# Optimization experiments

Measured on AMD Instinct MI355X. Metric: run time of the kernel, lower is better.

Reference implementation:

```python
import jax, jax.numpy as jnp
import numpy as np

H = 150  # hidden per direction

def _lstm_dir(x, w_ih, w_hh, b_ih, b_hh):
    # x: [B, T, D] -> hs: [B, T, H]; PyTorch gate order i,f,g,o
    B = x.shape[0]
    xg = jnp.einsum('btd,gd->btg', x, w_ih) + b_ih + b_hh  # precompute input projection [B,T,4H]
    def step(carry, xt):
        h, c = carry
        g = xt + h @ w_hh.T
        i, f, gg, o = jnp.split(g, 4, axis=-1)
        i, f, o = jax.nn.sigmoid(i), jax.nn.sigmoid(f), jax.nn.sigmoid(o)
        c = f * c + i * jnp.tanh(gg)
        h = o * jnp.tanh(c)
        return (h, c), h
    init = (jnp.zeros((B, H), x.dtype), jnp.zeros((B, H), x.dtype))
    _, hs = jax.lax.scan(step, init, jnp.swapaxes(xg, 0, 1))  # [T,B,H]
    return jnp.swapaxes(hs, 0, 1)

def _bilstm(x, w_ih_f, w_hh_f, b_ih_f, b_hh_f, w_ih_b, w_hh_b, b_ih_b, b_hh_b):
    fwd = _lstm_dir(x, w_ih_f, w_hh_f, b_ih_f, b_hh_f)
    bwd = jnp.flip(_lstm_dir(jnp.flip(x, axis=1), w_ih_b, w_hh_b, b_ih_b, b_hh_b), axis=1)
    return jnp.concatenate([fwd, bwd], axis=-1)  # [B, T, 2H]

def setup_inputs() -> dict:
    key = jax.random.key(0)
    ks = jax.random.split(key, 20)
    s = 0.05
    d = {
        'sentences': jax.random.normal(ks[0], (1024, 128, 343), jnp.float32),
        'w_ih_f1': jax.random.normal(ks[1], (600, 343)) * s,
        'w_hh_f1': jax.random.normal(ks[2], (600, 150)) * s,
        'b_ih_f1': jax.random.normal(ks[3], (600,)) * s,
        'b_hh_f1': jax.random.normal(ks[4], (600,)) * s,
        'w_ih_b1': jax.random.normal(ks[5], (600, 343)) * s,
        'w_hh_b1': jax.random.normal(ks[6], (600, 150)) * s,
        'b_ih_b1': jax.random.normal(ks[7], (600,)) * s,
        'b_hh_b1': jax.random.normal(ks[8], (600,)) * s,
        'w_ih_f2': jax.random.normal(ks[9], (600, 300)) * s,
        'w_hh_f2': jax.random.normal(ks[10], (600, 150)) * s,
        'b_ih_f2': jax.random.normal(ks[11], (600,)) * s,
        'b_hh_f2': jax.random.normal(ks[12], (600,)) * s,
        'w_ih_b2': jax.random.normal(ks[13], (600, 300)) * s,
        'w_hh_b2': jax.random.normal(ks[14], (600, 150)) * s,
        'b_ih_b2': jax.random.normal(ks[15], (600,)) * s,
        'b_hh_b2': jax.random.normal(ks[16], (600,)) * s,
        'w_out': jax.random.normal(ks[17], (7, 300)) * s,
        'b_out': jax.random.normal(ks[18], (7,)) * s,
    }
    return d

def reference(sentences, w_ih_f1, w_hh_f1, b_ih_f1, b_hh_f1, w_ih_b1, w_hh_b1, b_ih_b1, b_hh_b1,
              w_ih_f2, w_hh_f2, b_ih_f2, b_hh_f2, w_ih_b2, w_hh_b2, b_ih_b2, b_hh_b2, w_out, b_out):
    # Layer 1: per-sentence BiLSTM over words, batched instead of a python loop (dropout is eval-mode identity)
    word_out = _bilstm(sentences, w_ih_f1, w_hh_f1, b_ih_f1, b_hh_f1, w_ih_b1, w_hh_b1, b_ih_b1, b_hh_b1)  # [S,T,300]
    sent_emb = jnp.max(word_out, axis=1)  # max-pool over words -> [S,300]
    # Layer 2: BiLSTM over the sequence of sentence embeddings (batch of 1 paragraph)
    sent_out = _bilstm(sent_emb[None], w_ih_f2, w_hh_f2, b_ih_f2, b_hh_f2, w_ih_b2, w_hh_b2, b_ih_b2, b_hh_b2)[0]  # [S,300]
    log_probs = jax.nn.log_softmax(sent_out @ w_out.T + b_out, axis=-1)  # [S,7]
    return log_probs
```

## Files before the change

### kernel.cpp

```cpp
#include <hip/hip_runtime.h>
#include <hip/hip_bf16.h>
#include <hip/hip_fp16.h>

typedef short bf16x8 __attribute__((ext_vector_type(8)));
typedef float f32x4 __attribute__((ext_vector_type(4)));
typedef unsigned short u16x4 __attribute__((ext_vector_type(4)));
typedef unsigned int uint32;

#define MFMA_B16(a,b,c) __builtin_amdgcn_mfma_f32_16x16x32_bf16(a,b,c,0,0,0)

#define NS   1024
#define TLEN 128
#define DD   343
#define HH   150
#define GG   600
#define KX   352
#define XR   360
#define HR   168
#define KXP  44
#define NP   640
#define NG2  640

#define OFF_WXP  0u
#define OFF_WHP  901120u
#define OFF_B1   1310720u
#define OFF_W2B  1315840u
#define OFF_W2I  1725440u
#define OFF_SE   3184640u
#define OFF_XG2  4413440u
#define OFF_H2O  9656320u
#define OFF_XBF  10885120u
#define NEED_BF  103159808ull
#define OFF_XG1  103159808ull

#define PE0 450560
#define PE1 655360
#define PE2 656640
#define PE3 861440
#define PE4 1226240

__device__ __forceinline__ float rcp_fast(float x) { return __builtin_amdgcn_rcpf(x); }
__device__ __forceinline__ float sigm(float x) { return rcp_fast(1.f + __expf(-x)); }
__device__ __forceinline__ float tanh_fast(float x) { return 1.f - 2.f * rcp_fast(__expf(2.f * x) + 1.f); }

typedef __attribute__((address_space(1))) const void GASV;
typedef __attribute__((address_space(3))) void LASV;
__device__ __forceinline__ void gload_lds16(const void* g, void* l) {
  __builtin_amdgcn_global_load_lds((GASV*)g, (LASV*)l, 16, 0, 0);
}

__device__ __forceinline__ void bar_lds() {
  asm volatile("s_waitcnt lgkmcnt(0)" ::: "memory");
  __builtin_amdgcn_s_barrier();
  asm volatile("" ::: "memory");
}
__device__ __forceinline__ void bar_full() {
  asm volatile("s_waitcnt vmcnt(0) lgkmcnt(0)" ::: "memory");
  __builtin_amdgcn_s_barrier();
  asm volatile("" ::: "memory");
}

__device__ __forceinline__ unsigned short f2bu(float v) {
  __hip_bfloat16 b = __float2bfloat16(v);
  return __builtin_bit_cast(unsigned short, b);
}

__global__ __launch_bounds__(256) void prep_kernel(
    const float* __restrict__ wif1, const float* __restrict__ whf1,
    const float* __restrict__ bif1, const float* __restrict__ bhf1,
    const float* __restrict__ wib1, const float* __restrict__ whb1,
    const float* __restrict__ bib1, const float* __restrict__ bhb1,
    const float* __restrict__ wif2, const float* __restrict__ wib2,
    const float* __restrict__ whf2, const float* __restrict__ whb2,
    __hip_bfloat16* __restrict__ WXp, __hip_bfloat16* __restrict__ WHp,
    float* __restrict__ B1, __hip_bfloat16* __restrict__ W2B, float* __restrict__ W2I)
{
  int i = blockIdx.x * 256 + threadIdx.x;
  if (i < PE0) {
    int d = i / 225280; int r = i - d * 225280;
    int p = r / 5120;   int r2 = r - p * 5120;
    int n2 = r2 >> 3;   int jj = r2 & 7;
    int k = p * 8 + jj;
    int g = n2 / 160, j = n2 - g * 160;
    const float* w = d ? wib1 : wif1;
    float v = (j < HH && k < DD) ? w[(g * HH + j) * DD + k] : 0.f;
    WXp[i] = __float2bfloat16(v);
  } else if (i < PE1) {
    int ii = i - PE0;
    int d = ii / 102400; int r = ii - d * 102400;
    int p = r / 5120;    int r2 = r - p * 5120;
    int n2 = r2 >> 3;    int jj = r2 & 7;
    int k = p * 8 + jj;
    int g = n2 / 160, j = n2 - g * 160;
    const float* w = d ? whb1 : whf1;
    float v = (j < HH && k < HH) ? w[(g * HH + j) * HH + k] : 0.f;
    WHp[ii] = __float2bfloat16(v);
  } else if (i < PE2) {
    int ii = i - PE1;
    int d = ii / NP; int n2 = ii - d * NP;
    int g = n2 / 160, j = n2 - g * 160;
    float v = 0.f;
    if (j < HH) {
      int n = g * HH + j;
      v = d ? (bib1[n] + bhb1[n]) : (bif1[n] + bhf1[n]);
    }
    B1[ii] = v;
  } else if (i < PE3) {
    int ii = i - PE2;
    int d = ii / 102400; int r = ii - d * 102400;
    int n2 = r / 160;    int k = r - n2 * 160;
    int g = n2 / 160, j = n2 - g * 160;
    const float* w = d ? whb2 : whf2;
    float v = (j < HH && k < HH) ? w[(g * HH + j) * HH + k] : 0.f;
    W2B[ii] = __float2bfloat16(v);
  } else if (i < PE4) {
    int ii = i - PE3;
    int d = ii / 182400; int r = ii - d * 182400;
    int k = r / 608;     int n = r - k * 608;
    const float* w = d ? wib2 : wif2;
    float v = (n < GG) ? w[n * 300 + k] : 0.f;
    W2I[ii] = v;
  }
}

__global__ __launch_bounds__(256) void xcvt_kernel(
    const float* __restrict__ x, __hip_bfloat16* __restrict__ XBF)
{
  const int total4 = NS * TLEN * (KX / 4);
  for (int idx = blockIdx.x * 256 + threadIdx.x; idx < total4; idx += gridDim.x * 256) {
    int row = idx / 88;
    int c4 = (idx - row * 88) * 4;
    const float* src = x + (size_t)row * DD + c4;
    float v0 = 0.f, v1 = 0.f, v2 = 0.f, v3 = 0.f;
    if (c4 + 3 < DD) {
      v0 = __builtin_nontemporal_load(src);
      v1 = __builtin_nontemporal_load(src + 1);
      v2 = __builtin_nontemporal_load(src + 2);
      v3 = __builtin_nontemporal_load(src + 3);
    } else {
      if (c4 < DD)     v0 = src[0];
      if (c4 + 1 < DD) v1 = src[1];
      if (c4 + 2 < DD) v2 = src[2];
    }
    u16x4 o;
    o.x = f2bu(v0); o.y = f2bu(v1); o.z = f2bu(v2); o.w = f2bu(v3);
    *(u16x4*)((unsigned short*)XBF + (size_t)row * KX + c4) = o;
  }
}

#define GA_SMEM (64u * 720u)

__global__ __launch_bounds__(512) void xg1_gemm(
    const __hip_bfloat16* __restrict__ XBF, const __hip_bfloat16* __restrict__ WXp,
    const float* __restrict__ B1, __hip_bfloat16* __restrict__ XG1,
    int sBase, int CS)
{
  extern __shared__ char smem[];
  __hip_bfloat16* xsA = (__hip_bfloat16*)smem;

  const int bid = blockIdx.x;
  const int dir = bid & 1;
  const int mh = (bid >> 1) & 1;
  const int mtl = bid >> 2;
  const int sg = sBase + mtl;

  const int tid = threadIdx.x;
  const int lane = tid & 63;
  const int wv = tid >> 6;
  const int wr = wv >> 2;
  const int wc = wv & 3;
  const int c16 = lane & 15;
  const int kgrp = lane >> 4;

  #pragma unroll
  for (int i = 0; i < 8; ++i) {
    int rid = wv * 8 + i;
    if (lane < 44) {
      const __hip_bfloat16* gp = XBF + ((size_t)sg * TLEN + mh * 64 + rid) * KX + lane * 8;
      gload_lds16((const void*)gp, (void*)(smem + rid * 720));
    }
  }
  bar_full();

  const __hip_bfloat16* WXd = WXp + (size_t)dir * KXP * NP * 8;
  __hip_bfloat16* outd = XG1 + ((size_t)dir * CS + mtl) * TLEN * NG2;

  #pragma unroll
  for (int nh = 0; nh < 2; ++nh) {
    const int nbase = nh * 320 + wc * 80;
    f32x4 acc[2][5];
    #pragma unroll
    for (int mi = 0; mi < 2; ++mi)
      #pragma unroll
      for (int nf = 0; nf < 5; ++nf) acc[mi][nf] = (f32x4){0.f, 0.f, 0.f, 0.f};

    for (int kk = 0; kk < 11; ++kk) {
      bf16x8 a[2], b[5];
      #pragma unroll
      for (int mi = 0; mi < 2; ++mi)
        a[mi] = *reinterpret_cast<const bf16x8*>(
            xsA + (wr * 32 + mi * 16 + c16) * XR + kk * 32 + kgrp * 8);
      #pragma unroll
      for (int nf = 0; nf < 5; ++nf)
        b[nf] = *reinterpret_cast<const bf16x8*>(
            WXd + ((size_t)(kk * 4 + kgrp) * NP + nbase + nf * 16 + c16) * 8);
      #pragma unroll
      for (int mi = 0; mi < 2; ++mi)
        #pragma unroll
        for (int nf = 0; nf < 5; ++nf)
          acc[mi][nf] = MFMA_B16(a[mi], b[nf], acc[mi][nf]);
    }

    float bias[5];
    #pragma unroll
    for (int nf = 0; nf < 5; ++nf)
      bias[nf] = B1[dir * NP + nbase + nf * 16 + c16];

    #pragma unroll
    for (int mi = 0; mi < 2; ++mi)
      #pragma unroll
      for (int r = 0; r < 4; ++r) {
        int t = mh * 64 + wr * 32 + mi * 16 + kgrp * 4 + r;
        __hip_bfloat16* row = outd + (size_t)t * NG2;
        #pragma unroll
        for (int nf = 0; nf < 5; ++nf)
          row[nbase + nf * 16 + c16] = __float2bfloat16(acc[mi][nf][r] + bias[nf]);
      }
  }
}

__global__ __launch_bounds__(640) void lstm1_rec(
    const __hip_bfloat16* __restrict__ XG1, const __hip_bfloat16* __restrict__ WHp,
    float* __restrict__ SE, int sBase, int CS)
{
  __shared__ __hip_bfloat16 hs[16 * HR];

  const int tid = threadIdx.x;
  const int lane = tid & 63;
  const int wv = tid >> 6;
  const int dir = blockIdx.x & 1;
  const int grp = blockIdx.x >> 1;
  const int cls0 = grp * 8;
  const int s0g = sBase + cls0;
  const int c16 = lane & 15;
  const int kgrp = lane >> 4;
  const int j = wv * 16 + c16;

  for (int e = tid; e < 16 * HR; e += 640) hs[e] = __float2bfloat16(0.f);

  const __hip_bfloat16* WHd = WHp + (size_t)dir * 20 * NP * 8;
  bf16x8 whr[5][4];
  #pragma unroll
  for (int kh = 0; kh < 5; ++kh)
    #pragma unroll
    for (int g4 = 0; g4 < 4; ++g4) {
      whr[kh][g4] = *reinterpret_cast<const bf16x8*>(
          WHd + ((size_t)(kh * 4 + kgrp) * NP + g4 * 160 + j) * 8);
      asm volatile("" : "+v"(whr[kh][g4]));
    }

  float creg[4] = {0.f, 0.f, 0.f, 0.f};
  float mxr[4] = {-3e38f, -3e38f, -3e38f, -3e38f};

  const __hip_bfloat16* xgd = XG1 + (size_t)dir * CS * TLEN * NG2;
  const int sentb = cls0 + (kgrp & 1) * 4;
  const int par = kgrp >> 1;

  float xq[16], xqN[16];
  #pragma unroll
  for (int g4 = 0; g4 < 4; ++g4)
    #pragma unroll
    for (int r = 0; r < 4; ++r) {
      int tt = dir ? (127 - par) : par;
      xq[g4 * 4 + r] = __bfloat162float(
          xgd[((size_t)(sentb + r) * TLEN + tt) * NG2 + g4 * 160 + j]);
    }
  __syncthreads();

  for (int p = 0; p < 64; ++p) {
    f32x4 acc[4];
    #pragma unroll
    for (int g4 = 0; g4 < 4; ++g4) {
      acc[g4][0] = xq[g4 * 4 + 0]; acc[g4][1] = xq[g4 * 4 + 1];
      acc[g4][2] = xq[g4 * 4 + 2]; acc[g4][3] = xq[g4 * 4 + 3];
    }
    if (p < 63) {
      #pragma unroll
      for (int g4 = 0; g4 < 4; ++g4)
        #pragma unroll
        for (int r = 0; r < 4; ++r) {
          int tl = 2 * (p + 1) + par;
          int tt = dir ? (127 - tl) : tl;
          xqN[g4 * 4 + r] = __bfloat162float(
              xgd[((size_t)(sentb + r) * TLEN + tt) * NG2 + g4 * 160 + j]);
        }
    }
    #pragma unroll
    for (int kh = 0; kh < 5; ++kh) {
      bf16x8 ah = *reinterpret_cast<const bf16x8*>(hs + c16 * HR + kh * 32 + kgrp * 8);
      #pragma unroll
      for (int g4 = 0; g4 < 4; ++g4)
        acc[g4] = MFMA_B16(ah, whr[kh][g4], acc[g4]);
    }
    {
      const bool act = (kgrp < 2);
      #pragma unroll
      for (int r = 0; r < 4; ++r) {
        float iv = sigm(acc[0][r]);
        float fv = sigm(acc[1][r]);
        float gv = tanh_fast(acc[2][r]);
        float ov = sigm(acc[3][r]);
        float cin = __shfl_xor(creg[r], 32);
        float cn = fv * cin + iv * gv;
        float h = ov * tanh_fast(cn);
        creg[r] = act ? cn : creg[r];
        mxr[r] = act ? fmaxf(mxr[r], h) : mxr[r];
        if (act) hs[(8 + kgrp * 4 + r) * HR + j] = __float2bfloat16(h);
      }
    }
    bar_lds();
    #pragma unroll
    for (int kh = 0; kh < 5; ++kh) {
      bf16x8 ah = *reinterpret_cast<const bf16x8*>(hs + c16 * HR + kh * 32 + kgrp * 8);
      #pragma unroll
      for (int g4 = 0; g4 < 4; ++g4)
        acc[g4] = MFMA_B16(ah, whr[kh][g4], acc[g4]);
    }
    {
      const bool act = (kgrp >= 2);
      #pragma unroll
      for (int r = 0; r < 4; ++r) {
        float iv = sigm(acc[0][r]);
        float fv = sigm(acc[1][r]);
        float gv = tanh_fast(acc[2][r]);
        float ov = sigm(acc[3][r]);
        float cin = __shfl_xor(creg[r], 32);
        float cn = fv * cin + iv * gv;
        float h = ov * tanh_fast(cn);
        creg[r] = act ? cn : creg[r];
        mxr[r] = act ? fmaxf(mxr[r], h) : mxr[r];
        if (act) {
          int s = (kgrp - 2) * 4 + r;
          hs[s * HR + j] = __float2bfloat16(h);
          hs[(8 + s) * HR + j] = __float2bfloat16(0.f);
        }
      }
    }
    bar_lds();
    #pragma unroll
    for (int q = 0; q < 16; ++q) xq[q] = xqN[q];
  }

  #pragma unroll
  for (int r = 0; r < 4; ++r) {
    float m = fmaxf(mxr[r], __shfl_xor(mxr[r], 32));
    if (kgrp < 2 && j < HH)
      SE[(size_t)(s0g + kgrp * 4 + r) * 300 + dir * HH + j] = m;
  }
}

__global__ __launch_bounds__(256, 1) void xg2_kernel(
    const float* __restrict__ SE, const float* __restrict__ W2I,
    const float* __restrict__ bif2, const float* __restrict__ bhf2,
    const float* __restrict__ bib2, const float* __restrict__ bhb2,
    float* __restrict__ XG2)
{
  __shared__ float se[32 * 304];
  const int d = blockIdx.x >> 5, st = blockIdx.x & 31, sb = st * 32;
  const int tid = threadIdx.x;
  for (int e = tid; e < 32 * 300; e += 256) {
    int si = e / 300, k = e - si * 300;
    se[si * 304 + k] = SE[(size_t)(sb + si) * 300 + k];
  }
  __syncthreads();
  for (int pass = 0; pass < 3; ++pass) {
    int n = pass * 256 + tid;
    if (n < GG) {
      int n2 = (n / 150) * 160 + (n % 150);
      float bias = d ? (bib2[n] + bhb2[n]) : (bif2[n] + bhf2[n]);
      float acc[32];
      #pragma unroll
      for (int si = 0; si < 32; ++si) acc[si] = bias;
      const float* wcol = W2I + (size_t)d * 300 * 608 + n;
      for (int k = 0; k < 300; ++k) {
        float wvv = wcol[(size_t)k * 608];
        #pragma unroll
        for (int si = 0; si < 32; ++si) acc[si] += wvv * se[si * 304 + k];
      }
      #pragma unroll
      for (int si = 0; si < 32; ++si)
        XG2[((size_t)d * NS + sb + si) * NG2 + n2] = acc[si];
    }
  }
  for (int e = tid; e < 32 * 40; e += 256) {
    int si = e / 40, q = e - si * 40;
    int g = q / 10, jp = 150 + (q - g * 10);
    XG2[((size_t)d * NS + sb + si) * NG2 + g * 160 + jp] = 0.f;
  }
}

__global__ __launch_bounds__(640) void lstm2_kernel(
    const __hip_bfloat16* __restrict__ W2B, const float* __restrict__ XG2,
    float* __restrict__ H2O)
{
  const int dir = blockIdx.x;
  const int tid = threadIdx.x;
  const int lane = tid & 63;
  const int wv = tid >> 6;
  const int c16 = lane & 15;
  const int kg = lane >> 4;
  const int j = wv * 16 + c16;
  __shared__ __align__(16) __hip_bfloat16 hbuf[2][160];

  const f32x4 ZERO4 = {0.f, 0.f, 0.f, 0.f};

  const __hip_bfloat16* Wd = W2B + (size_t)dir * NP * 160;
  bf16x8 wf[5][4];
  #pragma unroll
  for (int kt = 0; kt < 5; ++kt)
    #pragma unroll
    for (int g4 = 0; g4 < 4; ++g4) {
      wf[kt][g4] = *reinterpret_cast<const bf16x8*>(
          Wd + (size_t)(g4 * 160 + j) * 160 + kt * 32 + kg * 8);
      asm volatile("" : "+v"(wf[kt][g4]));
    }

  if (tid < 160) hbuf[0][tid] = __float2bfloat16(0.f);
  __syncthreads();

  float creg = 0.f;
  const float* xg = XG2 + (size_t)dir * NS * NG2;

  float xqA[16], xqB[16];
  #pragma unroll
  for (int q = 0; q < 4; ++q)
    #pragma unroll
    for (int g4 = 0; g4 < 4; ++g4) {
      int ss2 = dir ? (1023 - q) : q;
      xqA[q * 4 + g4] = xg[(size_t)ss2 * NG2 + g4 * 160 + j];
    }

  for (int grp = 0; grp < 256; ++grp) {
    #pragma unroll
    for (int q = 0; q < 4; ++q)
      #pragma unroll
      for (int g4 = 0; g4 < 4; ++g4) {
        int sl = grp * 4 + 4 + q;
        if (sl < 1024) {
          int ss2 = dir ? (1023 - sl) : sl;
          xqB[q * 4 + g4] = xg[(size_t)ss2 * NG2 + g4 * 160 + j];
        } else {
          xqB[q * 4 + g4] = 0.f;
        }
      }
    #pragma unroll
    for (int q = 0; q < 4; ++q) {
      const int step = grp * 4 + q;
      const int ss = dir ? (1023 - step) : step;
      const int par = q & 1;
      bf16x8 hf[5];
      #pragma unroll
      for (int kt = 0; kt < 5; ++kt)
        hf[kt] = *reinterpret_cast<const bf16x8*>(&hbuf[par][kt * 32 + kg * 8]);
      __builtin_amdgcn_s_setprio(1);
      f32x4 aA[4], aB[4];
      #pragma unroll
      for (int g4 = 0; g4 < 4; ++g4) {
        aA[g4] = MFMA_B16(hf[0], wf[0][g4], ZERO4);
        aB[g4] = MFMA_B16(hf[1], wf[1][g4], ZERO4);
      }
      #pragma unroll
      for (int g4 = 0; g4 < 4; ++g4) {
        aA[g4] = MFMA_B16(hf[2], wf[2][g4], aA[g4]);
        aB[g4] = MFMA_B16(hf[3], wf[3][g4], aB[g4]);
        aA[g4] = MFMA_B16(hf[4], wf[4][g4], aA[g4]);
      }
      __builtin_amdgcn_s_setprio(0);
      float iv = sigm(aA[0][0] + aB[0][0] + xqA[q * 4 + 0]);
      float fv = sigm(aA[1][0] + aB[1][0] + xqA[q * 4 + 1]);
      float gv = tanh_fast(aA[2][0] + aB[2][0] + xqA[q * 4 + 2]);
      float ov = sigm(aA[3][0] + aB[3][0] + xqA[q * 4 + 3]);
      creg = fv * creg + iv * gv;
      float nh = ov * tanh_fast(creg);
      if (kg == 0) {
        hbuf[par ^ 1][j] = __float2bfloat16(nh);
        if (j < HH) H2O[(size_t)ss * 300 + dir * HH + j] = nh;
      }
      bar_lds();
    }
    #pragma unroll
    for (int q = 0; q < 16; ++q) xqA[q] = xqB[q];
  }
}

__global__ __launch_bounds__(256, 1) void head_kernel(
    const float* __restrict__ H2O, const float* __restrict__ w_out,
    const float* __restrict__ b_out, float* __restrict__ out)
{
  int s = blockIdx.x * 256 + threadIdx.x;
  if (s >= NS) return;
  float acc[7];
  #pragma unroll
  for (int c = 0; c < 7; ++c) acc[c] = b_out[c];
  const float* hrow = H2O + (size_t)s * 300;
  for (int k = 0; k < 300; ++k) {
    float hv = hrow[k];
    #pragma unroll
    for (int c = 0; c < 7; ++c) acc[c] += hv * w_out[c * 300 + k];
  }
  float m = acc[0];
  #pragma unroll
  for (int c = 1; c < 7; ++c) m = fmaxf(m, acc[c]);
  float sum = 0.f;
  #pragma unroll
  for (int c = 0; c < 7; ++c) sum += __expf(acc[c] - m);
  float lse = m + __logf(sum);
  #pragma unroll
  for (int c = 0; c < 7; ++c) out[s * 7 + c] = acc[c] - lse;
}

extern "C" void kernel_launch(void* const* d_in, const int* in_sizes, int n_in,
                              void* d_out, int out_size, void* d_ws, size_t ws_size,
                              hipStream_t stream) {
  const float* x      = (const float*)d_in[0];
  const float* wif1   = (const float*)d_in[1];
  const float* whf1   = (const float*)d_in[2];
  const float* bif1   = (const float*)d_in[3];
  const float* bhf1   = (const float*)d_in[4];
  const float* wib1   = (const float*)d_in[5];
  const float* whb1   = (const float*)d_in[6];
  const float* bib1   = (const float*)d_in[7];
  const float* bhb1   = (const float*)d_in[8];
  const float* wif2   = (const float*)d_in[9];
  const float* whf2   = (const float*)d_in[10];
  const float* bif2   = (const float*)d_in[11];
  const float* bhf2   = (const float*)d_in[12];
  const float* wib2   = (const float*)d_in[13];
  const float* whb2   = (const float*)d_in[14];
  const float* bib2   = (const float*)d_in[15];
  const float* bhb2   = (const float*)d_in[16];
  const float* w_out  = (const float*)d_in[17];
  const float* b_out  = (const float*)d_in[18];

  char* ws = (char*)d_ws;
  __hip_bfloat16* WXp = (__hip_bfloat16*)(ws + OFF_WXP);
  __hip_bfloat16* WHp = (__hip_bfloat16*)(ws + OFF_WHP);
  float*    B1  = (float*)(ws + OFF_B1);
  __hip_bfloat16* W2B = (__hip_bfloat16*)(ws + OFF_W2B);
  float*    W2I = (float*)(ws + OFF_W2I);
  float*    SE  = (float*)(ws + OFF_SE);
  float*    XG2 = (float*)(ws + OFF_XG2);
  float*    H2O = (float*)(ws + OFF_H2O);
  __hip_bfloat16* XBF = (__hip_bfloat16*)(ws + OFF_XBF);
  __hip_bfloat16* XG1 = (__hip_bfloat16*)(ws + OFF_XG1);

  const bool useBF = (ws_size >= NEED_BF);

  int CS = 0;
  if (useBF && ws_size >= NEED_BF + 128ull * 327680ull) {
    size_t avail = ws_size - NEED_BF;
    CS = 1024;
    while ((size_t)CS * 327680ull > avail) CS >>= 1;
  }

  prep_kernel<<<(PE4 + 255) / 256, 256, 0, stream>>>(
      wif1, whf1, bif1, bhf1, wib1, whb1, bib1, bhb1,
      wif2, wib2, whf2, whb2, WXp, WHp, B1, W2B, W2I);

  if (useBF)
    xcvt_kernel<<<4096, 256, 0, stream>>>(x, XBF);

  if (CS > 0) {
    (void)hipFuncSetAttribute((const void*)xg1_gemm,
                              hipFuncAttributeMaxDynamicSharedMemorySize, GA_SMEM);
    for (int sBase = 0; sBase < NS; sBase += CS) {
      xg1_gemm<<<4 * CS, 512, GA_SMEM, stream>>>(XBF, WXp, B1, XG1, sBase, CS);
      lstm1_rec<<<CS / 4, 640, 0, stream>>>(XG1, WHp, SE, sBase, CS);
    }
  } else {
    for (int sBase = 0; sBase < NS; sBase += 0) { break; }
  }

  xg2_kernel<<<64, 256, 0, stream>>>(SE, W2I, bif2, bhf2, bib2, bhb2, XG2);

  lstm2_kernel<<<2, 640, 0, stream>>>(W2B, XG2, H2O);

  head_kernel<<<4, 256, 0, stream>>>(H2O, w_out, b_out, (float*)d_out);
}
```

Measured before the change: 1.410 ms.

## Fuse fp32-to-bf16 input conversion into xg1 GEMM and retile per sentence

Removes the separate xcvt kernel and its bf16 staging buffer. Each xg1_gemm block now converts one whole sentence (128 rows) from fp32 straight into LDS and computes both directions, so the input is read once and the A tile is reused across directions. The workspace requirement shrinks accordingly. The lstm2 loop also changes from 4-step to 2-step prefetch groups and drops the setprio hints. The trade-off is fewer, larger blocks that do scalar fp32 loads instead of async global-to-LDS copies, and higher register use from a 4x5 accumulator tile.

```diff
diff --git a/kernel.cpp b/kernel.cpp
--- a/kernel.cpp
+++ b/kernel.cpp
@@ -29,9 +29,7 @@
 #define OFF_SE   3184640u
 #define OFF_XG2  4413440u
 #define OFF_H2O  9656320u
-#define OFF_XBF  10885120u
-#define NEED_BF  103159808ull
-#define OFF_XG1  103159808ull
+#define OFF_XG1  10885120ull
 
 #define PE0 450560
 #define PE1 655360
@@ -43,19 +41,8 @@
 __device__ __forceinline__ float sigm(float x) { return rcp_fast(1.f + __expf(-x)); }
 __device__ __forceinline__ float tanh_fast(float x) { return 1.f - 2.f * rcp_fast(__expf(2.f * x) + 1.f); }
 
-typedef __attribute__((address_space(1))) const void GASV;
-typedef __attribute__((address_space(3))) void LASV;
-__device__ __forceinline__ void gload_lds16(const void* g, void* l) {
-  __builtin_amdgcn_global_load_lds((GASV*)g, (LASV*)l, 16, 0, 0);
-}
-
 __device__ __forceinline__ void bar_lds() {
   asm volatile("s_waitcnt lgkmcnt(0)" ::: "memory");
-  __builtin_amdgcn_s_barrier();
-  asm volatile("" ::: "memory");
-}
-__device__ __forceinline__ void bar_full() {
-  asm volatile("s_waitcnt vmcnt(0) lgkmcnt(0)" ::: "memory");
   __builtin_amdgcn_s_barrier();
   asm volatile("" ::: "memory");
 }
@@ -123,45 +110,17 @@
   }
 }
 
-__global__ __launch_bounds__(256) void xcvt_kernel(
-    const float* __restrict__ x, __hip_bfloat16* __restrict__ XBF)
-{
-  const int total4 = NS * TLEN * (KX / 4);
-  for (int idx = blockIdx.x * 256 + threadIdx.x; idx < total4; idx += gridDim.x * 256) {
-    int row = idx / 88;
-    int c4 = (idx - row * 88) * 4;
-    const float* src = x + (size_t)row * DD + c4;
-    float v0 = 0.f, v1 = 0.f, v2 = 0.f, v3 = 0.f;
-    if (c4 + 3 < DD) {
-      v0 = __builtin_nontemporal_load(src);
-      v1 = __builtin_nontemporal_load(src + 1);
-      v2 = __builtin_nontemporal_load(src + 2);
-      v3 = __builtin_nontemporal_load(src + 3);
-    } else {
-      if (c4 < DD)     v0 = src[0];
-      if (c4 + 1 < DD) v1 = src[1];
-      if (c4 + 2 < DD) v2 = src[2];
-    }
-    u16x4 o;
-    o.x = f2bu(v0); o.y = f2bu(v1); o.z = f2bu(v2); o.w = f2bu(v3);
-    *(u16x4*)((unsigned short*)XBF + (size_t)row * KX + c4) = o;
-  }
-}
-
-#define GA_SMEM (64u * 720u)
+#define GA_SMEM (128u * 720u)
 
 __global__ __launch_bounds__(512) void xg1_gemm(
-    const __hip_bfloat16* __restrict__ XBF, const __hip_bfloat16* __restrict__ WXp,
+    const float* __restrict__ x, const __hip_bfloat16* __restrict__ WXp,
     const float* __restrict__ B1, __hip_bfloat16* __restrict__ XG1,
     int sBase, int CS)
 {
   extern __shared__ char smem[];
   __hip_bfloat16* xsA = (__hip_bfloat16*)smem;
 
-  const int bid = blockIdx.x;
-  const int dir = bid & 1;
-  const int mh = (bid >> 1) & 1;
-  const int mtl = bid >> 2;
+  const int mtl = blockIdx.x;
   const int sg = sBase + mtl;
 
   const int tid = threadIdx.x;
@@ -172,60 +131,69 @@
   const int c16 = lane & 15;
   const int kgrp = lane >> 4;
 
-  #pragma unroll
-  for (int i = 0; i < 8; ++i) {
-    int rid = wv * 8 + i;
-    if (lane < 44) {
-      const __hip_bfloat16* gp = XBF + ((size_t)sg * TLEN + mh * 64 + rid) * KX + lane * 8;
-      gload_lds16((const void*)gp, (void*)(smem + rid * 720));
-    }
-  }
-  bar_full();
-
-  const __hip_bfloat16* WXd = WXp + (size_t)dir * KXP * NP * 8;
-  __hip_bfloat16* outd = XG1 + ((size_t)dir * CS + mtl) * TLEN * NG2;
-
-  #pragma unroll
-  for (int nh = 0; nh < 2; ++nh) {
-    const int nbase = nh * 320 + wc * 80;
-    f32x4 acc[2][5];
-    #pragma unroll
-    for (int mi = 0; mi < 2; ++mi)
-      #pragma unroll
-      for (int nf = 0; nf < 5; ++nf) acc[mi][nf] = (f32x4){0.f, 0.f, 0.f, 0.f};
-
-    for (int kk = 0; kk < 11; ++kk) {
-      bf16x8 a[2], b[5];
-      #pragma unroll
-      for (int mi = 0; mi < 2; ++mi)
-        a[mi] = *reinterpret_cast<const bf16x8*>(
-            xsA + (wr * 32 + mi * 16 + c16) * XR + kk * 32 + kgrp * 8);
+  for (int g = tid; g < 11264; g += 512) {
+    int row = g / 88;
+    int c4 = (g - row * 88) * 4;
+    const float* src = x + ((size_t)sg * TLEN + row) * DD + c4;
+    float v0 = 0.f, v1 = 0.f, v2 = 0.f, v3 = 0.f;
+    if (c4 + 3 < DD) { v0 = src[0]; v1 = src[1]; v2 = src[2]; v3 = src[3]; }
+    else {
+      if (c4 < DD)     v0 = src[0];
+      if (c4 + 1 < DD) v1 = src[1];
+      if (c4 + 2 < DD) v2 = src[2];
+    }
+    u16x4 o;
+    o.x = f2bu(v0); o.y = f2bu(v1); o.z = f2bu(v2); o.w = f2bu(v3);
+    *(u16x4*)(smem + row * 720 + c4 * 2) = o;
+  }
+  bar_lds();
+
+  for (int dir = 0; dir < 2; ++dir) {
+    const __hip_bfloat16* WXd = WXp + (size_t)dir * KXP * NP * 8;
+    __hip_bfloat16* outd = XG1 + ((size_t)dir * CS + mtl) * TLEN * NG2;
+
+    #pragma unroll
+    for (int nh = 0; nh < 2; ++nh) {
+      const int nbase = nh * 320 + wc * 80;
+      f32x4 acc[4][5];
+      #pragma unroll
+      for (int mi = 0; mi < 4; ++mi)
+        #pragma unroll
+        for (int nf = 0; nf < 5; ++nf) acc[mi][nf] = (f32x4){0.f, 0.f, 0.f, 0.f};
+
+      for (int kk = 0; kk < 11; ++kk) {
+        bf16x8 a[4], b[5];
+        #pragma unroll
+        for (int mi = 0; mi < 4; ++mi)
+          a[mi] = *reinterpret_cast<const bf16x8*>(
+              xsA + (wr * 64 + mi * 16 + c16) * XR + kk * 32 + kgrp * 8);
+        #pragma unroll
+        for (int nf = 0; nf < 5; ++nf)
+          b[nf] = *reinterpret_cast<const bf16x8*>(
+              WXd + ((size_t)(kk * 4 + kgrp) * NP + nbase + nf * 16 + c16) * 8);
+        #pragma unroll
+        for (int mi = 0; mi < 4; ++mi)
+          #pragma unroll
+          for (int nf = 0; nf < 5; ++nf)
+            acc[mi][nf] = MFMA_B16(a[mi], b[nf], acc[mi][nf]);
+      }
+
+      float bias[5];
       #pragma unroll
       for (int nf = 0; nf < 5; ++nf)
-        b[nf] = *reinterpret_cast<const bf16x8*>(
-            WXd + ((size_t)(kk * 4 + kgrp) * NP + nbase + nf * 16 + c16) * 8);
-      #pragma unroll
-      for (int mi = 0; mi < 2; ++mi)
-        #pragma unroll
-        for (int nf = 0; nf < 5; ++nf)
-          acc[mi][nf] = MFMA_B16(a[mi], b[nf], acc[mi][nf]);
-    }
-
-    float bias[5];
-    #pragma unroll
-    for (int nf = 0; nf < 5; ++nf)
-      bias[nf] = B1[dir * NP + nbase + nf * 16 + c16];
-
-    #pragma unroll
-    for (int mi = 0; mi < 2; ++mi)
-      #pragma unroll
-      for (int r = 0; r < 4; ++r) {
-        int t = mh * 64 + wr * 32 + mi * 16 + kgrp * 4 + r;
-        __hip_bfloat16* row = outd + (size_t)t * NG2;
-        #pragma unroll
-        for (int nf = 0; nf < 5; ++nf)
-          row[nbase + nf * 16 + c16] = __float2bfloat16(acc[mi][nf][r] + bias[nf]);
-      }
+        bias[nf] = B1[dir * NP + nbase + nf * 16 + c16];
+
+      #pragma unroll
+      for (int mi = 0; mi < 4; ++mi)
+        #pragma unroll
+        for (int r = 0; r < 4; ++r) {
+          int t = wr * 64 + mi * 16 + kgrp * 4 + r;
+          __hip_bfloat16* row = outd + (size_t)t * NG2;
+          #pragma unroll
+          for (int nf = 0; nf < 5; ++nf)
+            row[nbase + nf * 16 + c16] = __float2bfloat16(acc[mi][nf][r] + bias[nf]);
+        }
+    }
   }
 }
 
@@ -431,38 +399,36 @@
   float creg = 0.f;
   const float* xg = XG2 + (size_t)dir * NS * NG2;
 
-  float xqA[16], xqB[16];
-  #pragma unroll
-  for (int q = 0; q < 4; ++q)
+  float xqC[8], xqN[8];
+  #pragma unroll
+  for (int q = 0; q < 2; ++q)
     #pragma unroll
     for (int g4 = 0; g4 < 4; ++g4) {
       int ss2 = dir ? (1023 - q) : q;
-      xqA[q * 4 + g4] = xg[(size_t)ss2 * NG2 + g4 * 160 + j];
-    }
-
-  for (int grp = 0; grp < 256; ++grp) {
-    #pragma unroll
-    for (int q = 0; q < 4; ++q)
+      xqC[q * 4 + g4] = xg[(size_t)ss2 * NG2 + g4 * 160 + j];
+    }
+
+  for (int grp = 0; grp < 512; ++grp) {
+    #pragma unroll
+    for (int q = 0; q < 2; ++q)
       #pragma unroll
       for (int g4 = 0; g4 < 4; ++g4) {
-        int sl = grp * 4 + 4 + q;
+        int sl = grp * 2 + 2 + q;
         if (sl < 1024) {
           int ss2 = dir ? (1023 - sl) : sl;
-          xqB[q * 4 + g4] = xg[(size_t)ss2 * NG2 + g4 * 160 + j];
+          xqN[q * 4 + g4] = xg[(size_t)ss2 * NG2 + g4 * 160 + j];
         } else {
-          xqB[q * 4 + g4] = 0.f;
+          xqN[q * 4 + g4] = 0.f;
         }
       }
     #pragma unroll
-    for (int q = 0; q < 4; ++q) {
-      const int step = grp * 4 + q;
+    for (int q = 0; q < 2; ++q) {
+      const int step = grp * 2 + q;
       const int ss = dir ? (1023 - step) : step;
-      const int par = q & 1;
       bf16x8 hf[5];
       #pragma unroll
       for (int kt = 0; kt < 5; ++kt)
-        hf[kt] = *reinterpret_cast<const bf16x8*>(&hbuf[par][kt * 32 + kg * 8]);
-      __builtin_amdgcn_s_setprio(1);
+        hf[kt] = *reinterpret_cast<const bf16x8*>(&hbuf[q][kt * 32 + kg * 8]);
       f32x4 aA[4], aB[4];
       #pragma unroll
       for (int g4 = 0; g4 < 4; ++g4) {
@@ -475,21 +441,20 @@
         aB[g4] = MFMA_B16(hf[3], wf[3][g4], aB[g4]);
         aA[g4] = MFMA_B16(hf[4], wf[4][g4], aA[g4]);
       }
-      __builtin_amdgcn_s_setprio(0);
-      float iv = sigm(aA[0][0] + aB[0][0] + xqA[q * 4 + 0]);
-      float fv = sigm(aA[1][0] + aB[1][0] + xqA[q * 4 + 1]);
-      float gv = tanh_fast(aA[2][0] + aB[2][0] + xqA[q * 4 + 2]);
-      float ov = sigm(aA[3][0] + aB[3][0] + xqA[q * 4 + 3]);
+      float iv = sigm(aA[0][0] + aB[0][0] + xqC[q * 4 + 0]);
+      float fv = sigm(aA[1][0] + aB[1][0] + xqC[q * 4 + 1]);
+      float gv = tanh_fast(aA[2][0] + aB[2][0] + xqC[q * 4 + 2]);
+      float ov = sigm(aA[3][0] + aB[3][0] + xqC[q * 4 + 3]);
       creg = fv * creg + iv * gv;
       float nh = ov * tanh_fast(creg);
       if (kg == 0) {
-        hbuf[par ^ 1][j] = __float2bfloat16(nh);
+        hbuf[q ^ 1][j] = __float2bfloat16(nh);
         if (j < HH) H2O[(size_t)ss * 300 + dir * HH + j] = nh;
       }
       bar_lds();
     }
     #pragma unroll
-    for (int q = 0; q < 16; ++q) xqA[q] = xqB[q];
+    for (int q = 0; q < 8; ++q) xqC[q] = xqN[q];
   }
 }
 
@@ -551,34 +516,24 @@
   float*    SE  = (float*)(ws + OFF_SE);
   float*    XG2 = (float*)(ws + OFF_XG2);
   float*    H2O = (float*)(ws + OFF_H2O);
-  __hip_bfloat16* XBF = (__hip_bfloat16*)(ws + OFF_XBF);
   __hip_bfloat16* XG1 = (__hip_bfloat16*)(ws + OFF_XG1);
 
-  const bool useBF = (ws_size >= NEED_BF);
-
-  int CS = 0;
-  if (useBF && ws_size >= NEED_BF + 128ull * 327680ull) {
-    size_t avail = ws_size - NEED_BF;
+  int CS = 128;
+  if (ws_size > OFF_XG1) {
+    size_t avail = ws_size - OFF_XG1;
     CS = 1024;
-    while ((size_t)CS * 327680ull > avail) CS >>= 1;
+    while (CS > 128 && (size_t)CS * 327680ull > avail) CS >>= 1;
   }
 
   prep_kernel<<<(PE4 + 255) / 256, 256, 0, stream>>>(
       wif1, whf1, bif1, bhf1, wib1, whb1, bib1, bhb1,
       wif2, wib2, whf2, whb2, WXp, WHp, B1, W2B, W2I);
 
-  if (useBF)
-    xcvt_kernel<<<4096, 256, 0, stream>>>(x, XBF);
-
-  if (CS > 0) {
-    (void)hipFuncSetAttribute((const void*)xg1_gemm,
-                              hipFuncAttributeMaxDynamicSharedMemorySize, GA_SMEM);
-    for (int sBase = 0; sBase < NS; sBase += CS) {
-      xg1_gemm<<<4 * CS, 512, GA_SMEM, stream>>>(XBF, WXp, B1, XG1, sBase, CS);
-      lstm1_rec<<<CS / 4, 640, 0, stream>>>(XG1, WHp, SE, sBase, CS);
-    }
-  } else {
-    for (int sBase = 0; sBase < NS; sBase += 0) { break; }
+  (void)hipFuncSetAttribute((const void*)xg1_gemm,
+                            hipFuncAttributeMaxDynamicSharedMemorySize, GA_SMEM);
+  for (int sBase = 0; sBase < NS; sBase += CS) {
+    xg1_gemm<<<CS, 512, GA_SMEM, stream>>>(x, WXp, B1, XG1, sBase, CS);
+    lstm1_rec<<<CS / 4, 640, 0, stream>>>(XG1, WHp, SE, sBase, CS);
   }
 
   xg2_kernel<<<64, 256, 0, stream>>>(SE, W2I, bif2, bhf2, bib2, bhb2, XG2);
```

Result: faster. 1.352 ms, median of 2 (-4.1%).
